# Optimization experiments

Hardware: AMD Instinct MI355X
Metric: run time of the kernel (lower is better)

## Reference

```python
import jax, jax.numpy as jnp
import numpy as np

IN_F, HID, OUT_F = 171, 1024, 171

def _cond_lst(condition_num, groundtruth_num, seq_len):
    num_cycles = seq_len // (condition_num + groundtruth_num) + 1
    lst = np.zeros((num_cycles, condition_num + groundtruth_num), dtype=np.float32)
    lst[:, :groundtruth_num] = 1.0
    return lst.reshape(-1)[:seq_len]

def setup_inputs() -> dict:
    key = jax.random.key(0)
    ks = jax.random.split(key, 16)
    s = 0.02
    inp = {
        'real_seq': jax.random.normal(ks[0], (128, 128, IN_F), jnp.float32),
        'W_ih1': jax.random.normal(ks[1], (4 * HID, IN_F), jnp.float32) * s,
        'W_hh1': jax.random.normal(ks[2], (4 * HID, HID), jnp.float32) * s,
        'b_ih1': jnp.zeros((4 * HID,), jnp.float32),
        'b_hh1': jnp.zeros((4 * HID,), jnp.float32),
        'W_ih2': jax.random.normal(ks[3], (4 * HID, HID), jnp.float32) * s,
        'W_hh2': jax.random.normal(ks[4], (4 * HID, HID), jnp.float32) * s,
        'b_ih2': jnp.zeros((4 * HID,), jnp.float32),
        'b_hh2': jnp.zeros((4 * HID,), jnp.float32),
        'W_ih3': jax.random.normal(ks[5], (4 * HID, HID), jnp.float32) * s,
        'W_hh3': jax.random.normal(ks[6], (4 * HID, HID), jnp.float32) * s,
        'b_ih3': jnp.zeros((4 * HID,), jnp.float32),
        'b_hh3': jnp.zeros((4 * HID,), jnp.float32),
        'W_dec': jax.random.normal(ks[7], (OUT_F, HID), jnp.float32) * s,
        'b_dec': jnp.zeros((OUT_F,), jnp.float32),
        'condition_num': 5,
        'groundtruth_num': 5,
    }
    return inp

def _lstm_cell(x, h, c, Wih, Whh, bih, bhh):
    # PyTorch LSTMCell: gates ordered i, f, g, o
    g = x @ Wih.T + bih + h @ Whh.T + bhh
    i, f, gg, o = jnp.split(g, 4, axis=-1)
    c2 = jax.nn.sigmoid(f) * c + jax.nn.sigmoid(i) * jnp.tanh(gg)
    h2 = jax.nn.sigmoid(o) * jnp.tanh(c2)
    return h2, c2

def reference(real_seq, W_ih1, W_hh1, b_ih1, b_hh1, W_ih2, W_hh2, b_ih2, b_hh2,
              W_ih3, W_hh3, b_ih3, b_hh3, W_dec, b_dec, condition_num, groundtruth_num):
    B, T, _ = real_seq.shape
    cond = jnp.asarray(_cond_lst(condition_num, groundtruth_num, T))  # [T], 1=use ground truth
    z = jnp.zeros((B, HID), jnp.float32)
    carry0 = (z, z, z, z, z, z, jnp.zeros((B, OUT_F), jnp.float32))
    xs = (jnp.swapaxes(real_seq, 0, 1), cond)  # time-major

    def step(carry, x):
        h0, h1, h2, c0, c1, c2, out_frame = carry
        frame, c_flag = x
        in_frame = jnp.where(c_flag > 0.5, frame, out_frame)
        h0, c0 = _lstm_cell(in_frame, h0, c0, W_ih1, W_hh1, b_ih1, b_hh1)
        h1, c1 = _lstm_cell(h0, h1, c1, W_ih2, W_hh2, b_ih2, b_hh2)
        h2, c2 = _lstm_cell(h1, h2, c2, W_ih3, W_hh3, b_ih3, b_hh3)
        out_frame = h2 @ W_dec.T + b_dec
        return (h0, h1, h2, c0, c1, c2, out_frame), out_frame

    _, out_seq = jax.lax.scan(step, carry0, xs)  # [T, B, OUT_F]
    return jnp.swapaxes(out_seq, 0, 1)  # [B, T, OUT_F]
```

## Files before the change

kernel.cpp:

```cpp
#include <hip/hip_runtime.h>

#define TT 128
#define INF 171

typedef _Float16 half8 __attribute__((ext_vector_type(8)));
typedef float floatx4 __attribute__((ext_vector_type(4)));
typedef unsigned short u16;

#define XBSZ 163840
#define HSZ  131072

__device__ __forceinline__ u16 f2h(float f){
  _Float16 h = (_Float16)f;
  return __builtin_bit_cast(u16, h);
}
__device__ __forceinline__ float sigm(float x){ return 1.f/(1.f+__expf(-x)); }
__device__ __forceinline__ float tanh_(float x){ return 1.f - 2.f/(__expf(2.f*x)+1.f); }

__device__ __forceinline__ void scat_coh(u16* buf, int nch, int b, int k, u16 v){
  u16* p = buf + (size_t)((((b>>4)*nch + (k>>5))*4 + ((k>>3)&3))*16 + (b&15))*8 + (k&7);
  unsigned int vv = v;
  asm volatile("global_store_short %0, %1, off sc0 sc1" :: "v"(p), "v"(vv) : "memory");
}
__device__ __forceinline__ void ld16_coh(half8& d, const u16* p){
  asm volatile("global_load_dwordx4 %0, %1, off sc0 sc1" : "=&v"(d) : "v"(p) : "memory");
}

__global__ __launch_bounds__(256) void prep_w1f(const float* __restrict__ Wih1,
    const float* __restrict__ Whh1, u16* __restrict__ Wf){
  int u = blockIdx.x*256 + threadIdx.x;
  int tile = u / 2560;
  int r = u - tile*2560;
  int kc = r >> 6, l = r & 63;
  int row = (tile>>6)*1024 + (tile&63)*16 + (l&15);
  int k0 = kc*32 + ((l>>4)<<3);
  half8 hv;
  #pragma unroll
  for (int e=0;e<8;e++){
    int k = k0+e;
    float w = 0.f;
    if (k < 171)       w = Wih1[(size_t)row*171 + k];
    else if (k < 1195) w = Whh1[(size_t)row*1024 + (k-171)];
    hv[e] = (_Float16)w;
  }
  *(half8*)&Wf[(size_t)(tile*40 + kc)*512 + (size_t)l*8] = hv;
}

__global__ __launch_bounds__(256) void prep_w23f(const float* __restrict__ Wih2,
    const float* __restrict__ Whh2, const float* __restrict__ Wih3,
    const float* __restrict__ Whh3, u16* __restrict__ W2f, u16* __restrict__ W3f){
  int u = blockIdx.x*256 + threadIdx.x;
  int tile = u >> 12;
  int r = u & 4095;
  int kc = r >> 6, l = r & 63;
  int row = (tile>>6)*1024 + (tile&63)*16 + (l&15);
  int k0 = kc*32 + ((l>>4)<<3);
  half8 h2, h3;
  #pragma unroll
  for (int e=0;e<8;e++){
    int k = k0+e;
    size_t si = (size_t)row*1024 + (k & 1023);
    h2[e] = (_Float16)((k < 1024) ? Wih2[si] : Whh2[si]);
    h3[e] = (_Float16)((k < 1024) ? Wih3[si] : Whh3[si]);
  }
  size_t base = (size_t)(tile*64 + kc)*512 + (size_t)l*8;
  *(half8*)&W2f[base] = h2;
  *(half8*)&W3f[base] = h3;
}

__global__ __launch_bounds__(256) void prep_wdecf(const float* __restrict__ Wdec,
    u16* __restrict__ Wdf){
  int u = blockIdx.x*256 + threadIdx.x;
  int tile = u / 2048;
  int r = u & 2047;
  int kc = r >> 6, l = r & 63;
  int row = tile*16 + (l&15);
  int k0 = kc*32 + ((l>>4)<<3);
  half8 hv;
  #pragma unroll
  for (int e=0;e<8;e++){
    int k = k0+e;
    hv[e] = (_Float16)((row < 171) ? Wdec[(size_t)row*1024 + k] : 0.f);
  }
  *(half8*)&Wdf[(size_t)(tile*32 + kc)*512 + (size_t)l*8] = hv;
}

__global__ __launch_bounds__(256) void prep_misc(
    const float* __restrict__ rseq, const int* __restrict__ gnp,
    const float* __restrict__ bih1, const float* __restrict__ bhh1,
    const float* __restrict__ bih2, const float* __restrict__ bhh2,
    const float* __restrict__ bih3, const float* __restrict__ bhh3,
    const float* __restrict__ bdec,
    u16* __restrict__ Xb1f, u16* __restrict__ Hf, float* __restrict__ cbuf,
    float* __restrict__ b1, float* __restrict__ b2, float* __restrict__ b3,
    float* __restrict__ bd, int* __restrict__ bar)
{
  size_t idx = (size_t)blockIdx.x*256 + threadIdx.x;
  if (idx < 327680){
    int q = (int)(idx / 163840);
    int rem = (int)(idx % 163840);
    int btile = rem / 20480;
    int r2 = rem % 20480;
    int kc = r2 >> 9, r3 = r2 & 511;
    int l = r3 >> 3, e = r3 & 7;
    int b = btile*16 + (l&15);
    int k = kc*32 + ((l>>4)<<3) + e;
    float v = 0.f;
    if (q==0 && k < 171 && *gnp > 0) v = rseq[(size_t)b*TT*INF + k];
    Xb1f[idx] = f2h(v);
    return;
  }
  idx -= 327680;
  if (idx < 786432){ Hf[idx] = 0; return; }
  idx -= 786432;
  if (idx < 393216){ cbuf[idx] = 0.f; return; }
  idx -= 393216;
  if (idx < 12288){
    int which = (int)(idx >> 12), j = (int)(idx & 4095);
    float v = (which==0)? (bih1[j]+bhh1[j]) : (which==1)? (bih2[j]+bhh2[j]) : (bih3[j]+bhh3[j]);
    ((which==0)?b1:(which==1)?b2:b3)[j] = v;
    return;
  }
  idx -= 12288;
  if (idx < 176){ bd[idx] = (idx < 171) ? bdec[idx] : 0.f; return; }
  idx -= 176;
  if (idx < 512) bar[idx] = 0;
}

__device__ __forceinline__ void gridbar(int* __restrict__ bar, int bId, int bc, int* s_dead){
  asm volatile("s_waitcnt vmcnt(0)" ::: "memory");
  __syncthreads();
  if (threadIdx.x == 0 && !(*s_dead)){
    int* c1  = &bar[(bId & 7) * 32];
    int* c0  = &bar[288];
    int* gen = &bar[320];
    bool released = false;
    int o1 = __hip_atomic_fetch_add(c1, 1, __ATOMIC_RELAXED, __HIP_MEMORY_SCOPE_AGENT);
    if ((o1 & 31) == 31){
      int o0 = __hip_atomic_fetch_add(c0, 1, __ATOMIC_RELAXED, __HIP_MEMORY_SCOPE_AGENT);
      if ((o0 & 7) == 7){
        __hip_atomic_fetch_add(gen, 1, __ATOMIC_RELAXED, __HIP_MEMORY_SCOPE_AGENT);
        released = true;
      }
    }
    if (!released){
      long long t0 = clock64();
      while (__hip_atomic_load(gen, __ATOMIC_RELAXED, __HIP_MEMORY_SCOPE_AGENT) < bc + 1){
        __builtin_amdgcn_s_sleep(2);
        if (clock64() - t0 > 30000000LL){ *s_dead = 1; break; }
      }
    }
  }
  __syncthreads();
}

template<int NC, int NBC>
__device__ __forceinline__ void stage(const u16* const* srcs, u16* XL, int tid){
  half8 v[NC*NBC];
  #pragma unroll
  for (int c=0;c<NC;c++){
    #pragma unroll
    for (int i=0;i<NBC;i++)
      ld16_coh(v[c*NBC+i], srcs[c] + (size_t)i*4096 + (size_t)tid*8);
  }
  asm volatile("s_waitcnt vmcnt(0)" ::: "memory");
  __builtin_amdgcn_sched_barrier(0);
  #pragma unroll
  for (int c=0;c<NC;c++){
    #pragma unroll
    for (int i=0;i<NBC;i++)
      *(half8*)&XL[(size_t)(c*NBC+i)*4096 + (size_t)tid*8] = v[c*NBC+i];
  }
}

template<int KHALF, int GS>
__device__ __forceinline__ void gemm_stream(const u16* __restrict__ wp,
    const u16* __restrict__ x0, const u16* __restrict__ x1,
    floatx4& a0, floatx4& a1)
{
  constexpr int NG = KHALF/GS;
  half8 W[2][GS];
  #pragma unroll
  for (int i=0;i<GS;i++)
    W[0][i] = *(const half8*)(wp + (size_t)i*512);
  #pragma unroll
  for (int g8=0; g8<NG; g8++){
    const int cur = g8 & 1, nxt = cur ^ 1;
    if (g8+1 < NG){
      const size_t off = (size_t)(g8+1)*GS*512;
      #pragma unroll
      for (int i=0;i<GS;i++)
        W[nxt][i] = *(const half8*)(wp + off + (size_t)i*512);
    }
    #pragma unroll
    for (int i=0;i<GS;i++){
      half8 xv0 = *(const half8*)(x0 + (size_t)(g8*GS+i)*512);
      half8 xv1 = *(const half8*)(x1 + (size_t)(g8*GS+i)*512);
      a0 = __builtin_amdgcn_mfma_f32_16x16x32_f16(W[cur][i], xv0, a0, 0,0,0);
      a1 = __builtin_amdgcn_mfma_f32_16x16x32_f16(W[cur][i], xv1, a1, 0,0,0);
    }
  }
}

__global__ void __launch_bounds__(512,2) acro_persist(
    const u16* __restrict__ W1f, const u16* __restrict__ W2f,
    const u16* __restrict__ W3f, const u16* __restrict__ Wdf,
    u16* __restrict__ Xb1f, u16* __restrict__ Hf,
    const float* __restrict__ b1, const float* __restrict__ b2,
    const float* __restrict__ b3, const float* __restrict__ bd,
    const float* __restrict__ rseq, float* __restrict__ out,
    const int* __restrict__ cnp, const int* __restrict__ gnp, int* __restrict__ bar)
{
  __shared__ u16 XL[65536];
  __shared__ float gb[8][16][33];
  __shared__ int s_dead;
  const int bId = (int)blockIdx.x;
  const int js = (bId & 7)*8 + ((bId >> 5) & 7);
  const int nq = (bId >> 3) & 3;
  const int tid = (int)threadIdx.x;
  const int w = tid >> 6, l = tid & 63;
  const int g = w >> 1, hf = w & 1;
  const int l15 = l & 15, lq = l >> 4;
  const int uu = tid >> 5, bq = tid & 31;
  const int jj = js*16 + uu, bgg = nq*32 + bq;
  if (tid == 0) s_dead = 0;
  const int gnv = *gnp;
  int P = *cnp + gnv; if (P < 1) P = 1;
  int bc = 0;

  u16* H0[2] = { Hf,          Hf + HSZ   };
  u16* H1[2] = { Hf + 2*HSZ,  Hf + 3*HSZ };
  u16* H2[2] = { Hf + 4*HSZ,  Hf + 5*HSZ };

  half8 W2r[32];
  {
    const u16* wp = W2f + ((size_t)(g*64 + js)*64 + (size_t)hf*32)*512 + (size_t)(l<<3);
    #pragma unroll
    for (int i=0;i<32;i++) W2r[i] = *(const half8*)(wp + (size_t)i*512);
  }
  const int dtile = bId >> 2, dq_ = bId & 3;
  const int oo = dtile*16 + uu;
  float bs1[4], bs2[4], bs3[4];
  #pragma unroll
  for (int q=0;q<4;q++){
    bs1[q] = b1[q*1024 + jj];
    bs2[q] = b2[q*1024 + jj];
    bs3[q] = b3[q*1024 + jj];
  }
  const float bdr = (bId < 44) ? bd[oo] : 0.f;
  float c0r = 0.f, c1r = 0.f, c2r = 0.f;

  __syncthreads();
  for (int t=0; t<TT; t++){
    const int pr = t & 1, nx = pr ^ 1;

    #pragma unroll
    for (int i=0;i<32;i++) asm volatile("" : "+v"(W2r[i]));

    {
      const u16* xb = Xb1f + (size_t)pr*XBSZ;
      const u16* srcs[2] = { xb + (size_t)(nq*2)*20480, xb + (size_t)(nq*2+1)*20480 };
      stage<2,5>(srcs, XL, tid);
      __syncthreads();
      const u16* wp = W1f + ((size_t)(g*64 + js)*40 + (size_t)hf*20)*512 + (size_t)(l<<3);
      const u16* x0 = XL + (size_t)hf*10240 + (size_t)(l<<3);
      const u16* x1 = x0 + 20480;
      floatx4 a0{}, a1{};
      gemm_stream<20,4>(wp, x0, x1, a0, a1);
      #pragma unroll
      for (int r=0;r<4;r++){
        gb[w][lq*4+r][l15]      = a0[r];
        gb[w][lq*4+r][16 + l15] = a1[r];
      }
      __syncthreads();
      {
        float gi = gb[0][uu][bq] + gb[1][uu][bq] + bs1[0];
        float gf = gb[2][uu][bq] + gb[3][uu][bq] + bs1[1];
        float gg = gb[4][uu][bq] + gb[5][uu][bq] + bs1[2];
        float go = gb[6][uu][bq] + gb[7][uu][bq] + bs1[3];
        float c = sigm(gf)*c0r + sigm(gi)*tanh_(gg);
        c0r = c;
        u16 hb = f2h(sigm(go)*tanh_(c));
        scat_coh(H0[pr], 32, bgg, jj, hb);
        scat_coh(Xb1f + (size_t)nx*XBSZ, 40, bgg, 171 + jj, hb);
      }
    }
    gridbar(bar, bId, bc, &s_dead); bc++;

    {
      const u16* xa = H0[pr];
      const u16* xh = H1[nx];
      const u16* srcs[4] = {
        xa + (size_t)(nq*2  )*16384, xa + (size_t)(nq*2+1)*16384,
        xh + (size_t)(nq*2  )*16384, xh + (size_t)(nq*2+1)*16384 };
      stage<4,4>(srcs, XL, tid);
      __syncthreads();
      const u16* x0 = XL + (size_t)hf*32768 + (size_t)(l<<3);
      const u16* x1 = x0 + 16384;
      floatx4 a0{}, a1{};
      #pragma unroll
      for (int i=0;i<32;i++){
        half8 xv0 = *(const half8*)(x0 + (size_t)i*512);
        half8 xv1 = *(const half8*)(x1 + (size_t)i*512);
        a0 = __builtin_amdgcn_mfma_f32_16x16x32_f16(W2r[i], xv0, a0, 0,0,0);
        a1 = __builtin_amdgcn_mfma_f32_16x16x32_f16(W2r[i], xv1, a1, 0,0,0);
      }
      #pragma unroll
      for (int r=0;r<4;r++){
        gb[w][lq*4+r][l15]      = a0[r];
        gb[w][lq*4+r][16 + l15] = a1[r];
      }
      __syncthreads();
      {
        float gi = gb[0][uu][bq] + gb[1][uu][bq] + bs2[0];
        float gf = gb[2][uu][bq] + gb[3][uu][bq] + bs2[1];
        float gg = gb[4][uu][bq] + gb[5][uu][bq] + bs2[2];
        float go = gb[6][uu][bq] + gb[7][uu][bq] + bs2[3];
        float c = sigm(gf)*c1r + sigm(gi)*tanh_(gg);
        c1r = c;
        u16 hb = f2h(sigm(go)*tanh_(c));
        scat_coh(H1[pr], 32, bgg, jj, hb);
      }
    }
    gridbar(bar, bId, bc, &s_dead); bc++;

    {
      const u16* xa = H1[pr];
      const u16* xh = H2[nx];
      const u16* srcs[4] = {
        xa + (size_t)(nq*2  )*16384, xa + (size_t)(nq*2+1)*16384,
        xh + (size_t)(nq*2  )*16384, xh + (size_t)(nq*2+1)*16384 };
      stage<4,4>(srcs, XL, tid);
      __syncthreads();
      const u16* wp = W3f + ((size_t)(g*64 + js)*64 + (size_t)hf*32)*512 + (size_t)(l<<3);
      const u16* x0 = XL + (size_t)hf*32768 + (size_t)(l<<3);
      const u16* x1 = x0 + 16384;
      floatx4 a0{}, a1{};
      gemm_stream<32,8>(wp, x0, x1, a0, a1);
      #pragma unroll
      for (int r=0;r<4;r++){
        gb[w][lq*4+r][l15]      = a0[r];
        gb[w][lq*4+r][16 + l15] = a1[r];
      }
      __syncthreads();
      {
        float gi = gb[0][uu][bq] + gb[1][uu][bq] + bs3[0];
        float gf = gb[2][uu][bq] + gb[3][uu][bq] + bs3[1];
        float gg = gb[4][uu][bq] + gb[5][uu][bq] + bs3[2];
        float go = gb[6][uu][bq] + gb[7][uu][bq] + bs3[3];
        float c = sigm(gf)*c2r + sigm(gi)*tanh_(gg);
        c2r = c;
        u16 hb = f2h(sigm(go)*tanh_(c));
        scat_coh(H2[pr], 32, bgg, jj, hb);
      }
    }
    gridbar(bar, bId, bc, &s_dead); bc++;

    if (bId < 44){
      const u16* srcs[2] = { H2[pr] + (size_t)(dq_*2)*16384, H2[pr] + (size_t)(dq_*2+1)*16384 };
      stage<2,4>(srcs, XL, tid);
      __syncthreads();
      const u16* wp = Wdf + (size_t)(dtile*32 + w*4)*512 + (size_t)(l<<3);
      const u16* x0 = XL + (size_t)(w*4)*512 + (size_t)(l<<3);
      const u16* x1 = x0 + 16384;
      floatx4 d0{}, d1{};
      #pragma unroll
      for (int i=0;i<4;i++){
        half8 wv  = *(const half8*)(wp + (size_t)i*512);
        half8 a0v = *(const half8*)(x0 + (size_t)i*512);
        half8 a1v = *(const half8*)(x1 + (size_t)i*512);
        d0 = __builtin_amdgcn_mfma_f32_16x16x32_f16(wv, a0v, d0, 0,0,0);
        d1 = __builtin_amdgcn_mfma_f32_16x16x32_f16(wv, a1v, d1, 0,0,0);
      }
      #pragma unroll
      for (int r=0;r<4;r++){
        gb[w][lq*4+r][l15]      = d0[r];
        gb[w][lq*4+r][16 + l15] = d1[r];
      }
      __syncthreads();
      const int nf = (((t+1) % P) < gnv) ? 1 : 0;
      if (oo < 171){
        float v = bdr;
        #pragma unroll
        for (int i=0;i<8;i++) v += gb[i][uu][bq];
        int b = dq_*32 + bq;
        out[((size_t)b*TT + t)*INF + oo] = v;
        if (t+1 < TT){
          float src = nf ? rseq[((size_t)b*TT + (t+1))*INF + oo] : v;
          scat_coh(Xb1f + (size_t)nx*XBSZ, 40, b, oo, f2h(src));
        }
      }
    }
    gridbar(bar, bId, bc, &s_dead); bc++;
  }
}

extern "C" void kernel_launch(void* const* d_in, const int* in_sizes, int n_in,
                              void* d_out, int out_size, void* d_ws, size_t ws_size,
                              hipStream_t stream)
{
  const float* rseq = (const float*)d_in[0];
  const float* Wih1 = (const float*)d_in[1];
  const float* Whh1 = (const float*)d_in[2];
  const float* bih1 = (const float*)d_in[3];
  const float* bhh1 = (const float*)d_in[4];
  const float* Wih2 = (const float*)d_in[5];
  const float* Whh2 = (const float*)d_in[6];
  const float* bih2 = (const float*)d_in[7];
  const float* bhh2 = (const float*)d_in[8];
  const float* Wih3 = (const float*)d_in[9];
  const float* Whh3 = (const float*)d_in[10];
  const float* bih3 = (const float*)d_in[11];
  const float* bhh3 = (const float*)d_in[12];
  const float* Wdec = (const float*)d_in[13];
  const float* bdec = (const float*)d_in[14];
  const int* cn = (const int*)d_in[15];
  const int* gn = (const int*)d_in[16];
  float* out = (float*)d_out;

  char* p = (char*)d_ws;
  auto take = [&](size_t n){ void* r = (void*)p; p += (n + 255) & ~(size_t)255; return r; };
  u16* W1f  = (u16*)take(5242880UL*2);
  u16* W2f  = (u16*)take(8388608UL*2);
  u16* W3f  = (u16*)take(8388608UL*2);
  u16* Wdf  = (u16*)take(180224UL*2);
  u16* Xb1f = (u16*)take(327680UL*2);
  u16* Hf   = (u16*)take(786432UL*2);
  float* cbuf = (float*)take(393216UL*4);
  float* b1 = (float*)take(4096*4);
  float* b2 = (float*)take(4096*4);
  float* b3 = (float*)take(4096*4);
  float* bd = (float*)take(176*4);
  int* bar  = (int*)take(512*4);
  if ((size_t)(p - (char*)d_ws) > ws_size) return;

  prep_w1f  <<<2560,256,0,stream>>>(Wih1, Whh1, W1f);
  prep_w23f <<<4096,256,0,stream>>>(Wih2, Whh2, Wih3, Whh3, W2f, W3f);
  prep_wdecf<<<88,  256,0,stream>>>(Wdec, Wdf);
  prep_misc <<<5939,256,0,stream>>>(rseq, gn, bih1,bhh1,bih2,bhh2,bih3,bhh3,bdec,
                                    Xb1f, Hf, cbuf, b1,b2,b3,bd, bar);

  acro_persist<<<256,512,0,stream>>>(W1f, W2f, W3f, Wdf, Xb1f, Hf,
                                     b1, b2, b3, bd, rseq, out, cn, gn, bar);
}
```

Measured before the change: 4.822 ms.

## Split grid barrier per batch quarter and prefetch recurrent inputs across barriers

The single global two-level barrier becomes independent barriers per batch quarter (nq), each with two 32-block halves, since every block only consumes activations for its own batch slice. The decoder is remapped so blocks handle their own batch quarter, keeping the dependency local. Loads of the recurrent hidden states (H1/H2 previous step, layer-1 input columns) are issued before the barrier so they overlap the wait. W2 register caching is dropped in favour of streaming, which trades register pressure for extra weight traffic.

```diff
diff --git a/kernel.cpp b/kernel.cpp
--- a/kernel.cpp
+++ b/kernel.cpp
@@ -9,6 +9,8 @@
 
 #define XBSZ 163840
 #define HSZ  131072
+
+#define WAITV(n) asm volatile("s_waitcnt vmcnt(" #n ")" ::: "memory")
 
 __device__ __forceinline__ u16 f2h(float f){
   _Float16 h = (_Float16)f;
@@ -24,6 +26,15 @@
 }
 __device__ __forceinline__ void ld16_coh(half8& d, const u16* p){
   asm volatile("global_load_dwordx4 %0, %1, off sc0 sc1" : "=&v"(d) : "v"(p) : "memory");
+}
+
+template<int NB>
+__device__ __forceinline__ void issue_pair(const u16* s0, const u16* s1,
+    half8* v, int tid, int beat0){
+  #pragma unroll
+  for (int i=0;i<NB;i++) ld16_coh(v[i],    s0 + (size_t)(beat0+i)*4096 + (size_t)tid*8);
+  #pragma unroll
+  for (int i=0;i<NB;i++) ld16_coh(v[NB+i], s1 + (size_t)(beat0+i)*4096 + (size_t)tid*8);
 }
 
 __global__ __launch_bounds__(256) void prep_w1f(const float* __restrict__ Wih1,
@@ -127,50 +138,27 @@
   if (idx < 512) bar[idx] = 0;
 }
 
-__device__ __forceinline__ void gridbar(int* __restrict__ bar, int bId, int bc, int* s_dead){
-  asm volatile("s_waitcnt vmcnt(0)" ::: "memory");
+__device__ __forceinline__ void gridbar(int* __restrict__ bar, int cls, int hv,
+                                        int bc, int* s_dead){
   __syncthreads();
   if (threadIdx.x == 0 && !(*s_dead)){
-    int* c1  = &bar[(bId & 7) * 32];
-    int* c0  = &bar[288];
-    int* gen = &bar[320];
+    int* arr = &bar[cls*64 + hv*32];
+    int* gen = &bar[256 + cls*32];
     bool released = false;
-    int o1 = __hip_atomic_fetch_add(c1, 1, __ATOMIC_RELAXED, __HIP_MEMORY_SCOPE_AGENT);
-    if ((o1 & 31) == 31){
-      int o0 = __hip_atomic_fetch_add(c0, 1, __ATOMIC_RELAXED, __HIP_MEMORY_SCOPE_AGENT);
-      if ((o0 & 7) == 7){
-        __hip_atomic_fetch_add(gen, 1, __ATOMIC_RELAXED, __HIP_MEMORY_SCOPE_AGENT);
-        released = true;
-      }
+    int o = __hip_atomic_fetch_add(arr, 1, __ATOMIC_RELAXED, __HIP_MEMORY_SCOPE_AGENT);
+    if ((o & 31) == 31){
+      int og = __hip_atomic_fetch_add(gen, 1, __ATOMIC_RELAXED, __HIP_MEMORY_SCOPE_AGENT);
+      released = (og & 1) == 1;
     }
     if (!released){
       long long t0 = clock64();
-      while (__hip_atomic_load(gen, __ATOMIC_RELAXED, __HIP_MEMORY_SCOPE_AGENT) < bc + 1){
+      while (__hip_atomic_load(gen, __ATOMIC_RELAXED, __HIP_MEMORY_SCOPE_AGENT) < 2*(bc+1)){
         __builtin_amdgcn_s_sleep(2);
         if (clock64() - t0 > 30000000LL){ *s_dead = 1; break; }
       }
     }
   }
   __syncthreads();
-}
-
-template<int NC, int NBC>
-__device__ __forceinline__ void stage(const u16* const* srcs, u16* XL, int tid){
-  half8 v[NC*NBC];
-  #pragma unroll
-  for (int c=0;c<NC;c++){
-    #pragma unroll
-    for (int i=0;i<NBC;i++)
-      ld16_coh(v[c*NBC+i], srcs[c] + (size_t)i*4096 + (size_t)tid*8);
-  }
-  asm volatile("s_waitcnt vmcnt(0)" ::: "memory");
-  __builtin_amdgcn_sched_barrier(0);
-  #pragma unroll
-  for (int c=0;c<NC;c++){
-    #pragma unroll
-    for (int i=0;i<NBC;i++)
-      *(half8*)&XL[(size_t)(c*NBC+i)*4096 + (size_t)tid*8] = v[c*NBC+i];
-  }
 }
 
 template<int KHALF, int GS>
@@ -217,6 +205,7 @@
   const int bId = (int)blockIdx.x;
   const int js = (bId & 7)*8 + ((bId >> 5) & 7);
   const int nq = (bId >> 3) & 3;
+  const int bh = (bId >> 5) & 1;
   const int tid = (int)threadIdx.x;
   const int w = tid >> 6, l = tid & 63;
   const int g = w >> 1, hf = w & 1;
@@ -232,14 +221,6 @@
   u16* H1[2] = { Hf + 2*HSZ,  Hf + 3*HSZ };
   u16* H2[2] = { Hf + 4*HSZ,  Hf + 5*HSZ };
 
-  half8 W2r[32];
-  {
-    const u16* wp = W2f + ((size_t)(g*64 + js)*64 + (size_t)hf*32)*512 + (size_t)(l<<3);
-    #pragma unroll
-    for (int i=0;i<32;i++) W2r[i] = *(const half8*)(wp + (size_t)i*512);
-  }
-  const int dtile = bId >> 2, dq_ = bId & 3;
-  const int oo = dtile*16 + uu;
   float bs1[4], bs2[4], bs3[4];
   #pragma unroll
   for (int q=0;q<4;q++){
@@ -247,20 +228,32 @@
     bs2[q] = b2[q*1024 + jj];
     bs3[q] = b3[q*1024 + jj];
   }
-  const float bdr = (bId < 44) ? bd[oo] : 0.f;
+  const float bdr = (js < 11) ? bd[js*16 + uu] : 0.f;
+  const int oo = js*16 + uu;
   float c0r = 0.f, c1r = 0.f, c2r = 0.f;
+
+  half8 pf1[8], pf2[8], pf3[8];
+  issue_pair<4>(Xb1f + (size_t)(nq*2  )*20480,
+                Xb1f + (size_t)(nq*2+1)*20480, pf1, tid, 1);
 
   __syncthreads();
   for (int t=0; t<TT; t++){
     const int pr = t & 1, nx = pr ^ 1;
 
-    #pragma unroll
-    for (int i=0;i<32;i++) asm volatile("" : "+v"(W2r[i]));
-
     {
       const u16* xb = Xb1f + (size_t)pr*XBSZ;
-      const u16* srcs[2] = { xb + (size_t)(nq*2)*20480, xb + (size_t)(nq*2+1)*20480 };
-      stage<2,5>(srcs, XL, tid);
+      half8 fr0, fr1;
+      ld16_coh(fr0, xb + (size_t)(nq*2  )*20480 + (size_t)tid*8);
+      ld16_coh(fr1, xb + (size_t)(nq*2+1)*20480 + (size_t)tid*8);
+      WAITV(0);
+      __builtin_amdgcn_sched_barrier(0);
+      *(half8*)&XL[(size_t)tid*8] = fr0;
+      *(half8*)&XL[(size_t)5*4096 + (size_t)tid*8] = fr1;
+      #pragma unroll
+      for (int i=0;i<4;i++){
+        *(half8*)&XL[(size_t)(1+i)*4096 + (size_t)tid*8] = pf1[i];
+        *(half8*)&XL[(size_t)(6+i)*4096 + (size_t)tid*8] = pf1[4+i];
+      }
       __syncthreads();
       const u16* wp = W1f + ((size_t)(g*64 + js)*40 + (size_t)hf*20)*512 + (size_t)(l<<3);
       const u16* x0 = XL + (size_t)hf*10240 + (size_t)(l<<3);
@@ -284,27 +277,28 @@
         scat_coh(H0[pr], 32, bgg, jj, hb);
         scat_coh(Xb1f + (size_t)nx*XBSZ, 40, bgg, 171 + jj, hb);
       }
-    }
-    gridbar(bar, bId, bc, &s_dead); bc++;
+      issue_pair<4>(H1[nx] + (size_t)(nq*2  )*16384,
+                    H1[nx] + (size_t)(nq*2+1)*16384, pf2, tid, 0);
+    }
+    WAITV(8);
+    gridbar(bar, nq, bh, bc, &s_dead); bc++;
 
     {
-      const u16* xa = H0[pr];
-      const u16* xh = H1[nx];
-      const u16* srcs[4] = {
-        xa + (size_t)(nq*2  )*16384, xa + (size_t)(nq*2+1)*16384,
-        xh + (size_t)(nq*2  )*16384, xh + (size_t)(nq*2+1)*16384 };
-      stage<4,4>(srcs, XL, tid);
-      __syncthreads();
+      half8 fr[8];
+      issue_pair<4>(H0[pr] + (size_t)(nq*2  )*16384,
+                    H0[pr] + (size_t)(nq*2+1)*16384, fr, tid, 0);
+      WAITV(0);
+      __builtin_amdgcn_sched_barrier(0);
+      #pragma unroll
+      for (int i=0;i<8;i++) *(half8*)&XL[(size_t)i*4096 + (size_t)tid*8] = fr[i];
+      #pragma unroll
+      for (int i=0;i<8;i++) *(half8*)&XL[32768 + (size_t)i*4096 + (size_t)tid*8] = pf2[i];
+      __syncthreads();
+      const u16* wp = W2f + ((size_t)(g*64 + js)*64 + (size_t)hf*32)*512 + (size_t)(l<<3);
       const u16* x0 = XL + (size_t)hf*32768 + (size_t)(l<<3);
       const u16* x1 = x0 + 16384;
       floatx4 a0{}, a1{};
-      #pragma unroll
-      for (int i=0;i<32;i++){
-        half8 xv0 = *(const half8*)(x0 + (size_t)i*512);
-        half8 xv1 = *(const half8*)(x1 + (size_t)i*512);
-        a0 = __builtin_amdgcn_mfma_f32_16x16x32_f16(W2r[i], xv0, a0, 0,0,0);
-        a1 = __builtin_amdgcn_mfma_f32_16x16x32_f16(W2r[i], xv1, a1, 0,0,0);
-      }
+      gemm_stream<32,8>(wp, x0, x1, a0, a1);
       #pragma unroll
       for (int r=0;r<4;r++){
         gb[w][lq*4+r][l15]      = a0[r];
@@ -321,16 +315,22 @@
         u16 hb = f2h(sigm(go)*tanh_(c));
         scat_coh(H1[pr], 32, bgg, jj, hb);
       }
-    }
-    gridbar(bar, bId, bc, &s_dead); bc++;
+      issue_pair<4>(H2[nx] + (size_t)(nq*2  )*16384,
+                    H2[nx] + (size_t)(nq*2+1)*16384, pf3, tid, 0);
+    }
+    WAITV(8);
+    gridbar(bar, nq, bh, bc, &s_dead); bc++;
 
     {
-      const u16* xa = H1[pr];
-      const u16* xh = H2[nx];
-      const u16* srcs[4] = {
-        xa + (size_t)(nq*2  )*16384, xa + (size_t)(nq*2+1)*16384,
-        xh + (size_t)(nq*2  )*16384, xh + (size_t)(nq*2+1)*16384 };
-      stage<4,4>(srcs, XL, tid);
+      half8 fr[8];
+      issue_pair<4>(H1[pr] + (size_t)(nq*2  )*16384,
+                    H1[pr] + (size_t)(nq*2+1)*16384, fr, tid, 0);
+      WAITV(0);
+      __builtin_amdgcn_sched_barrier(0);
+      #pragma unroll
+      for (int i=0;i<8;i++) *(half8*)&XL[(size_t)i*4096 + (size_t)tid*8] = fr[i];
+      #pragma unroll
+      for (int i=0;i<8;i++) *(half8*)&XL[32768 + (size_t)i*4096 + (size_t)tid*8] = pf3[i];
       __syncthreads();
       const u16* wp = W3f + ((size_t)(g*64 + js)*64 + (size_t)hf*32)*512 + (size_t)(l<<3);
       const u16* x0 = XL + (size_t)hf*32768 + (size_t)(l<<3);
@@ -354,13 +354,19 @@
         scat_coh(H2[pr], 32, bgg, jj, hb);
       }
     }
-    gridbar(bar, bId, bc, &s_dead); bc++;
-
-    if (bId < 44){
-      const u16* srcs[2] = { H2[pr] + (size_t)(dq_*2)*16384, H2[pr] + (size_t)(dq_*2+1)*16384 };
-      stage<2,4>(srcs, XL, tid);
-      __syncthreads();
-      const u16* wp = Wdf + (size_t)(dtile*32 + w*4)*512 + (size_t)(l<<3);
+    WAITV(0);
+    gridbar(bar, nq, bh, bc, &s_dead); bc++;
+
+    if (js < 11){
+      half8 fd[8];
+      issue_pair<4>(H2[pr] + (size_t)(nq*2  )*16384,
+                    H2[pr] + (size_t)(nq*2+1)*16384, fd, tid, 0);
+      WAITV(0);
+      __builtin_amdgcn_sched_barrier(0);
+      #pragma unroll
+      for (int i=0;i<8;i++) *(half8*)&XL[(size_t)i*4096 + (size_t)tid*8] = fd[i];
+      __syncthreads();
+      const u16* wp = Wdf + (size_t)(js*32 + w*4)*512 + (size_t)(l<<3);
       const u16* x0 = XL + (size_t)(w*4)*512 + (size_t)(l<<3);
       const u16* x1 = x0 + 16384;
       floatx4 d0{}, d1{};
@@ -383,15 +389,22 @@
         float v = bdr;
         #pragma unroll
         for (int i=0;i<8;i++) v += gb[i][uu][bq];
-        int b = dq_*32 + bq;
-        out[((size_t)b*TT + t)*INF + oo] = v;
+        out[((size_t)bgg*TT + t)*INF + oo] = v;
         if (t+1 < TT){
-          float src = nf ? rseq[((size_t)b*TT + (t+1))*INF + oo] : v;
-          scat_coh(Xb1f + (size_t)nx*XBSZ, 40, b, oo, f2h(src));
+          float src = nf ? rseq[((size_t)bgg*TT + (t+1))*INF + oo] : v;
+          scat_coh(Xb1f + (size_t)nx*XBSZ, 40, bgg, oo, f2h(src));
         }
       }
     }
-    gridbar(bar, bId, bc, &s_dead); bc++;
+    if (t+1 < TT){
+      const u16* xbn = Xb1f + (size_t)nx*XBSZ;
+      issue_pair<4>(xbn + (size_t)(nq*2  )*20480,
+                    xbn + (size_t)(nq*2+1)*20480, pf1, tid, 1);
+      WAITV(8);
+    } else {
+      WAITV(0);
+    }
+    gridbar(bar, nq, bh, bc, &s_dead); bc++;
   }
 }
 
```

New measurement: 4.451 ms. 7.7% less time.
